# Kernel optimization log

Measured on AMD Instinct MI355X. Metric: run time of the kernel, lower is better.

The kernel has to match this reference:

```python
import jax, jax.numpy as jnp
import numpy as np

OUT_H, OUT_W, STRIDE = 100, 100, 4  # hardcoded in the torch module


def _downsample(pc):
    # pc: (B, 3, H, W) -> permute to (B, H, W, 3), strided-subsample, flatten to (B, N, 3)
    pc = jnp.transpose(pc, (0, 2, 3, 1))
    pc = pc[:, : OUT_H * STRIDE : STRIDE, : OUT_W * STRIDE : STRIDE, :]
    return pc.reshape(pc.shape[0], OUT_H * OUT_W, 3)


def setup_inputs() -> dict:
    key = jax.random.key(0)
    k1, k2 = jax.random.split(key)
    B, H, W = 4, 400, 400
    return {
        "target_pc": jax.random.normal(k1, (B, 3, H, W), dtype=jnp.float32),
        "source_pc": jax.random.normal(k2, (B, 3, H, W), dtype=jnp.float32),
    }


def reference(target_pc, source_pc):
    t = _downsample(target_pc)  # (B, N, 3) query points
    s = _downsample(source_pc)  # (B, N, 3) reference points
    # Squared Euclidean distances (B, Nt, Ns); argmin is identical for L2 vs L2^2.
    d2 = (
        jnp.sum(t * t, axis=-1)[:, :, None]
        + jnp.sum(s * s, axis=-1)[:, None, :]
        - 2.0 * jnp.einsum("bnd,bmd->bnm", t, s)
    )
    idx = jnp.argmin(d2, axis=-1)  # (B, Nt): nearest source index for each target point
    nearest = jnp.take_along_axis(s, idx[..., None], axis=1)  # (B, Nt, 3)
    per_batch = jnp.mean((nearest - t) ** 2, axis=(1, 2))  # MSE per batch element
    return jnp.mean(per_batch)
```

## Files before the change

### kernel.cpp

```cpp
#include <hip/hip_runtime.h>


#define BATCH  4
#define NPTS   10000
#define NPAD   10240
#define H      400
#define W      400
#define STRIDE 4
#define OUTW   100
#define NC     16
#define CHUNK  625
#define TBLKS  10
#define BLOCK  256
#define TPT    4

__global__ void prep_kernel(const float* __restrict__ tgt,
                            const float* __restrict__ src,
                            float4* __restrict__ S4,
                            float4* __restrict__ T4) {
    int gid = blockIdx.x * blockDim.x + threadIdx.x;
    if (gid < BATCH * NPAD) {
        int b = gid / NPAD;
        int n = gid % NPAD;
        float4 v = make_float4(0.f, 0.f, 0.f, 0.f);
        if (n < NPTS) {
            int h = n / OUTW, w = n % OUTW;
            int base = ((b * 3) * H + h * STRIDE) * W + w * STRIDE;
            float x = tgt[base];
            float y = tgt[base + H * W];
            float z = tgt[base + 2 * H * W];
            v = make_float4(x, y, z, x * x + y * y + z * z);
        }
        T4[gid] = v;
    } else {
        int sid = gid - BATCH * NPAD;
        if (sid < BATCH * NPTS) {
            int b = sid / NPTS;
            int m = sid % NPTS;
            int h = m / OUTW, w = m % OUTW;
            int base = ((b * 3) * H + h * STRIDE) * W + w * STRIDE;
            float x = src[base];
            float y = src[base + H * W];
            float z = src[base + 2 * H * W];
            S4[sid] = make_float4(-2.f * x, -2.f * y, -2.f * z,
                                  x * x + y * y + z * z);
        }
    }
}

__global__ __launch_bounds__(BLOCK) void knn_kernel(
        const float4* __restrict__ S4,
        const float4* __restrict__ T4,
        float* __restrict__ M2) {
    __shared__ float4 lds[CHUNK];
    const int tblk = blockIdx.x;
    const int cblk = blockIdx.y;
    const int b    = blockIdx.z;
    const int tid  = threadIdx.x;

    const float4* sbase = S4 + b * NPTS + cblk * CHUNK;
    for (int i = tid; i < CHUNK; i += BLOCK) lds[i] = sbase[i];

    const int tbase = b * NPAD + tblk * (BLOCK * TPT) + tid;
    float tx[TPT], ty[TPT], tz[TPT], mn[TPT];
#pragma unroll
    for (int k = 0; k < TPT; k++) {
        float4 t = T4[tbase + k * BLOCK];
        tx[k] = t.x; ty[k] = t.y; tz[k] = t.z;
        mn[k] = 3.0e38f;
    }
    __syncthreads();

#pragma unroll 5
    for (int j = 0; j < CHUNK; j++) {
        float4 s = lds[j];
#pragma unroll
        for (int k = 0; k < TPT; k++) {
            float d = fmaf(tx[k], s.x, s.w);
            d = fmaf(ty[k], s.y, d);
            d = fmaf(tz[k], s.z, d);
            mn[k] = fminf(mn[k], d);
        }
    }

    float* obase = M2 + (cblk * BATCH + b) * NPAD + tblk * (BLOCK * TPT) + tid;
#pragma unroll
    for (int k = 0; k < TPT; k++) obase[k * BLOCK] = mn[k];
}

__global__ void reduce_kernel(const float* __restrict__ M2,
                              const float4* __restrict__ T4,
                              float* __restrict__ out) {
    __shared__ float red[BLOCK / 64];
    int gid = blockIdx.x * BLOCK + threadIdx.x;
    float val = 0.f;
    if (gid < BATCH * NPTS) {
        int b = gid / NPTS;
        int n = gid % NPTS;
        float m = 3.0e38f;
#pragma unroll
        for (int c = 0; c < NC; c++)
            m = fminf(m, M2[(c * BATCH + b) * NPAD + n]);
        float tt = T4[b * NPAD + n].w;
        val = fmaxf(m + tt, 0.f);
    }
#pragma unroll
    for (int off = 32; off > 0; off >>= 1)
        val += __shfl_down(val, off, 64);
    int lane = threadIdx.x & 63;
    int wave = threadIdx.x >> 6;
    if (lane == 0) red[wave] = val;
    __syncthreads();
    if (threadIdx.x == 0) {
        float s = 0.f;
        for (int wv = 0; wv < BLOCK / 64; wv++) s += red[wv];
        atomicAdd(out, s * (1.0f / (BATCH * NPTS * 3)));
    }
}

extern "C" void kernel_launch(void* const* d_in, const int* in_sizes, int n_in,
                              void* d_out, int out_size, void* d_ws, size_t ws_size,
                              hipStream_t stream) {
    const float* tgt = (const float*)d_in[0];
    const float* src = (const float*)d_in[1];
    float* out = (float*)d_out;

    char* ws = (char*)d_ws;
    float4* S4 = (float4*)ws;
    float4* T4 = (float4*)(ws + (size_t)BATCH * NPTS * 16);
    float*  M2 = (float*)(ws + (size_t)BATCH * NPTS * 16
                             + (size_t)BATCH * NPAD * 16);

    hipMemsetAsync(out, 0, sizeof(float), stream);

    int nprep = BATCH * NPAD + BATCH * NPTS;
    prep_kernel<<<(nprep + 255) / 256, 256, 0, stream>>>(tgt, src, S4, T4);

    knn_kernel<<<dim3(TBLKS, NC, BATCH), BLOCK, 0, stream>>>(S4, T4, M2);

    reduce_kernel<<<(BATCH * NPTS + BLOCK - 1) / BLOCK, BLOCK, 0, stream>>>(
        M2, T4, out);
}
```

Baseline: 107.3 us.

## Restructure KNN inner loop with v_min3, 8 points per thread, prefetched LDS

New measurement: 122.6 us. 14.3% more time.

```diff
diff --git a/kernel.cpp b/kernel.cpp
--- a/kernel.cpp
+++ b/kernel.cpp
@@ -10,9 +10,17 @@
 #define OUTW   100
 #define NC     16
 #define CHUNK  625
-#define TBLKS  10
-#define BLOCK  256
-#define TPT    4
+#define CPAD   628
+#define KBLOCK 64
+#define TPT    8
+#define TBLKS  20
+#define RBLOCK 256
+
+__device__ __forceinline__ float min3f(float a, float b, float c) {
+    float r;
+    asm("v_min3_f32 %0, %1, %2, %3" : "=v"(r) : "v"(a), "v"(b), "v"(c));
+    return r;
+}
 
 __global__ void prep_kernel(const float* __restrict__ tgt,
                             const float* __restrict__ src,
@@ -48,51 +56,69 @@
     }
 }
 
-__global__ __launch_bounds__(BLOCK) void knn_kernel(
+#define COMPUTE4(q0, q1, q2, q3)                                   \
+    _Pragma("unroll")                                              \
+    for (int k = 0; k < TPT; k++) {                                \
+        float d0 = fmaf(tx[k], q0.x, q0.w);                        \
+        d0 = fmaf(ty[k], q0.y, d0);                                \
+        d0 = fmaf(tz[k], q0.z, d0);                                \
+        float d1 = fmaf(tx[k], q1.x, q1.w);                        \
+        d1 = fmaf(ty[k], q1.y, d1);                                \
+        d1 = fmaf(tz[k], q1.z, d1);                                \
+        float d2 = fmaf(tx[k], q2.x, q2.w);                        \
+        d2 = fmaf(ty[k], q2.y, d2);                                \
+        d2 = fmaf(tz[k], q2.z, d2);                                \
+        float d3 = fmaf(tx[k], q3.x, q3.w);                        \
+        d3 = fmaf(ty[k], q3.y, d3);                                \
+        d3 = fmaf(tz[k], q3.z, d3);                                \
+        mn[k] = min3f(mn[k], min3f(d0, d1, d2), d3);               \
+    }
+
+__global__ __launch_bounds__(KBLOCK) void knn_kernel(
         const float4* __restrict__ S4,
         const float4* __restrict__ T4,
         float* __restrict__ M2) {
-    __shared__ float4 lds[CHUNK];
+    __shared__ float4 lds[CPAD];
     const int tblk = blockIdx.x;
     const int cblk = blockIdx.y;
     const int b    = blockIdx.z;
     const int tid  = threadIdx.x;
 
     const float4* sbase = S4 + b * NPTS + cblk * CHUNK;
-    for (int i = tid; i < CHUNK; i += BLOCK) lds[i] = sbase[i];
+    for (int i = tid; i < CHUNK; i += KBLOCK) lds[i] = sbase[i];
+    if (tid < CPAD - CHUNK) lds[CHUNK + tid] = make_float4(0.f, 0.f, 0.f, 3.0e38f);
 
-    const int tbase = b * NPAD + tblk * (BLOCK * TPT) + tid;
+    const int tbase = b * NPAD + tblk * (KBLOCK * TPT) + tid;
     float tx[TPT], ty[TPT], tz[TPT], mn[TPT];
 #pragma unroll
     for (int k = 0; k < TPT; k++) {
-        float4 t = T4[tbase + k * BLOCK];
+        float4 t = T4[tbase + k * KBLOCK];
         tx[k] = t.x; ty[k] = t.y; tz[k] = t.z;
         mn[k] = 3.0e38f;
     }
     __syncthreads();
 
-#pragma unroll 5
-    for (int j = 0; j < CHUNK; j++) {
-        float4 s = lds[j];
+    float4 c0 = lds[0], c1 = lds[1], c2 = lds[2], c3 = lds[3];
+    for (int j = 4; j < CPAD; j += 4) {
+        float4 n0 = lds[j + 0];
+        float4 n1 = lds[j + 1];
+        float4 n2 = lds[j + 2];
+        float4 n3 = lds[j + 3];
+        COMPUTE4(c0, c1, c2, c3)
+        c0 = n0; c1 = n1; c2 = n2; c3 = n3;
+    }
+    COMPUTE4(c0, c1, c2, c3)
+
+    float* obase = M2 + (cblk * BATCH + b) * NPAD + tblk * (KBLOCK * TPT) + tid;
 #pragma unroll
-        for (int k = 0; k < TPT; k++) {
-            float d = fmaf(tx[k], s.x, s.w);
-            d = fmaf(ty[k], s.y, d);
-            d = fmaf(tz[k], s.z, d);
-            mn[k] = fminf(mn[k], d);
-        }
-    }
-
-    float* obase = M2 + (cblk * BATCH + b) * NPAD + tblk * (BLOCK * TPT) + tid;
-#pragma unroll
-    for (int k = 0; k < TPT; k++) obase[k * BLOCK] = mn[k];
+    for (int k = 0; k < TPT; k++) obase[k * KBLOCK] = mn[k];
 }
 
 __global__ void reduce_kernel(const float* __restrict__ M2,
                               const float4* __restrict__ T4,
                               float* __restrict__ out) {
-    __shared__ float red[BLOCK / 64];
-    int gid = blockIdx.x * BLOCK + threadIdx.x;
+    __shared__ float red[RBLOCK / 64];
+    int gid = blockIdx.x * RBLOCK + threadIdx.x;
     float val = 0.f;
     if (gid < BATCH * NPTS) {
         int b = gid / NPTS;
@@ -113,7 +139,7 @@
     __syncthreads();
     if (threadIdx.x == 0) {
         float s = 0.f;
-        for (int wv = 0; wv < BLOCK / 64; wv++) s += red[wv];
+        for (int wv = 0; wv < RBLOCK / 64; wv++) s += red[wv];
         atomicAdd(out, s * (1.0f / (BATCH * NPTS * 3)));
     }
 }
@@ -134,10 +160,10 @@
     hipMemsetAsync(out, 0, sizeof(float), stream);
 
     int nprep = BATCH * NPAD + BATCH * NPTS;
-    prep_kernel<<<(nprep + 255) / 256, 256, 0, stream>>>(tgt, src, S4, T4);
+    prep_kernel<<<(nprep + RBLOCK - 1) / RBLOCK, RBLOCK, 0, stream>>>(tgt, src, S4, T4);
 
-    knn_kernel<<<dim3(TBLKS, NC, BATCH), BLOCK, 0, stream>>>(S4, T4, M2);
+    knn_kernel<<<dim3(TBLKS, NC, BATCH), KBLOCK, 0, stream>>>(S4, T4, M2);
 
-    reduce_kernel<<<(BATCH * NPTS + BLOCK - 1) / BLOCK, BLOCK, 0, stream>>>(
+    reduce_kernel<<<(BATCH * NPTS + RBLOCK - 1) / RBLOCK, RBLOCK, 0, stream>>>(
         M2, T4, out);
 }
```

## Drop LDS staging, read padded source chunks directly, use min3 with more targets per thread

Applied to the files above, without the earlier changes.

Result: slower. 124.5 us (+16.0%).

```diff
diff --git a/kernel.cpp b/kernel.cpp
--- a/kernel.cpp
+++ b/kernel.cpp
@@ -8,11 +8,19 @@
 #define W      400
 #define STRIDE 4
 #define OUTW   100
-#define NC     16
-#define CHUNK  625
-#define TBLKS  10
+#define NC     64
+#define CHUNK  157
+#define CPAD   160
 #define BLOCK  256
-#define TPT    4
+#define TPT    8
+#define TBLKS  5
+#define RBLOCK 256
+
+__device__ __forceinline__ float min3f(float a, float b, float c) {
+    float r;
+    asm("v_min3_f32 %0, %1, %2, %3" : "=v"(r) : "v"(a), "v"(b), "v"(c));
+    return r;
+}
 
 __global__ void prep_kernel(const float* __restrict__ tgt,
                             const float* __restrict__ src,
@@ -34,16 +42,23 @@
         T4[gid] = v;
     } else {
         int sid = gid - BATCH * NPAD;
-        if (sid < BATCH * NPTS) {
-            int b = sid / NPTS;
-            int m = sid % NPTS;
-            int h = m / OUTW, w = m % OUTW;
-            int base = ((b * 3) * H + h * STRIDE) * W + w * STRIDE;
-            float x = src[base];
-            float y = src[base + H * W];
-            float z = src[base + 2 * H * W];
-            S4[sid] = make_float4(-2.f * x, -2.f * y, -2.f * z,
-                                  x * x + y * y + z * z);
+        if (sid < BATCH * NC * CPAD) {
+            int b = sid / (NC * CPAD);
+            int r = sid % (NC * CPAD);
+            int c = r / CPAD;
+            int i = r % CPAD;
+            int m = c * CHUNK + i;
+            float4 v = make_float4(0.f, 0.f, 0.f, 3.0e38f);
+            if (i < CHUNK && m < NPTS) {
+                int h = m / OUTW, w = m % OUTW;
+                int base = ((b * 3) * H + h * STRIDE) * W + w * STRIDE;
+                float x = src[base];
+                float y = src[base + H * W];
+                float z = src[base + 2 * H * W];
+                v = make_float4(-2.f * x, -2.f * y, -2.f * z,
+                                x * x + y * y + z * z);
+            }
+            S4[sid] = v;
         }
     }
 }
@@ -52,14 +67,12 @@
         const float4* __restrict__ S4,
         const float4* __restrict__ T4,
         float* __restrict__ M2) {
-    __shared__ float4 lds[CHUNK];
     const int tblk = blockIdx.x;
     const int cblk = blockIdx.y;
     const int b    = blockIdx.z;
     const int tid  = threadIdx.x;
 
-    const float4* sbase = S4 + b * NPTS + cblk * CHUNK;
-    for (int i = tid; i < CHUNK; i += BLOCK) lds[i] = sbase[i];
+    const float4* sbase = S4 + (size_t)(b * NC + cblk) * CPAD;
 
     const int tbase = b * NPAD + tblk * (BLOCK * TPT) + tid;
     float tx[TPT], ty[TPT], tz[TPT], mn[TPT];
@@ -69,21 +82,33 @@
         tx[k] = t.x; ty[k] = t.y; tz[k] = t.z;
         mn[k] = 3.0e38f;
     }
-    __syncthreads();
 
-#pragma unroll 5
-    for (int j = 0; j < CHUNK; j++) {
-        float4 s = lds[j];
+    for (int j = 0; j < CPAD; j += 4) {
+        float4 sa = sbase[j + 0];
+        float4 sb = sbase[j + 1];
+        float4 sc = sbase[j + 2];
+        float4 sd = sbase[j + 3];
 #pragma unroll
         for (int k = 0; k < TPT; k++) {
-            float d = fmaf(tx[k], s.x, s.w);
-            d = fmaf(ty[k], s.y, d);
-            d = fmaf(tz[k], s.z, d);
-            mn[k] = fminf(mn[k], d);
+            float da = fmaf(tx[k], sa.x, sa.w);
+            da = fmaf(ty[k], sa.y, da);
+            da = fmaf(tz[k], sa.z, da);
+            float db = fmaf(tx[k], sb.x, sb.w);
+            db = fmaf(ty[k], sb.y, db);
+            db = fmaf(tz[k], sb.z, db);
+            float dc = fmaf(tx[k], sc.x, sc.w);
+            dc = fmaf(ty[k], sc.y, dc);
+            dc = fmaf(tz[k], sc.z, dc);
+            float dd = fmaf(tx[k], sd.x, sd.w);
+            dd = fmaf(ty[k], sd.y, dd);
+            dd = fmaf(tz[k], sd.z, dd);
+            mn[k] = min3f(mn[k], da, db);
+            mn[k] = min3f(mn[k], dc, dd);
         }
     }
 
-    float* obase = M2 + (cblk * BATCH + b) * NPAD + tblk * (BLOCK * TPT) + tid;
+    float* obase = M2 + (size_t)(cblk * BATCH + b) * NPAD
+                      + tblk * (BLOCK * TPT) + tid;
 #pragma unroll
     for (int k = 0; k < TPT; k++) obase[k * BLOCK] = mn[k];
 }
@@ -91,16 +116,16 @@
 __global__ void reduce_kernel(const float* __restrict__ M2,
                               const float4* __restrict__ T4,
                               float* __restrict__ out) {
-    __shared__ float red[BLOCK / 64];
-    int gid = blockIdx.x * BLOCK + threadIdx.x;
+    __shared__ float red[RBLOCK / 64];
+    int gid = blockIdx.x * RBLOCK + threadIdx.x;
     float val = 0.f;
     if (gid < BATCH * NPTS) {
         int b = gid / NPTS;
         int n = gid % NPTS;
         float m = 3.0e38f;
-#pragma unroll
+#pragma unroll 8
         for (int c = 0; c < NC; c++)
-            m = fminf(m, M2[(c * BATCH + b) * NPAD + n]);
+            m = fminf(m, M2[(size_t)(c * BATCH + b) * NPAD + n]);
         float tt = T4[b * NPAD + n].w;
         val = fmaxf(m + tt, 0.f);
     }
@@ -113,7 +138,7 @@
     __syncthreads();
     if (threadIdx.x == 0) {
         float s = 0.f;
-        for (int wv = 0; wv < BLOCK / 64; wv++) s += red[wv];
+        for (int wv = 0; wv < RBLOCK / 64; wv++) s += red[wv];
         atomicAdd(out, s * (1.0f / (BATCH * NPTS * 3)));
     }
 }
@@ -127,17 +152,17 @@
 
     char* ws = (char*)d_ws;
     float4* S4 = (float4*)ws;
-    float4* T4 = (float4*)(ws + (size_t)BATCH * NPTS * 16);
-    float*  M2 = (float*)(ws + (size_t)BATCH * NPTS * 16
+    float4* T4 = (float4*)(ws + (size_t)BATCH * NC * CPAD * 16);
+    float*  M2 = (float*)(ws + (size_t)BATCH * NC * CPAD * 16
                              + (size_t)BATCH * NPAD * 16);
 
     hipMemsetAsync(out, 0, sizeof(float), stream);
 
-    int nprep = BATCH * NPAD + BATCH * NPTS;
-    prep_kernel<<<(nprep + 255) / 256, 256, 0, stream>>>(tgt, src, S4, T4);
+    int nprep = BATCH * NPAD + BATCH * NC * CPAD;
+    prep_kernel<<<(nprep + RBLOCK - 1) / RBLOCK, RBLOCK, 0, stream>>>(tgt, src, S4, T4);
 
     knn_kernel<<<dim3(TBLKS, NC, BATCH), BLOCK, 0, stream>>>(S4, T4, M2);
 
-    reduce_kernel<<<(BATCH * NPTS + BLOCK - 1) / BLOCK, BLOCK, 0, stream>>>(
+    reduce_kernel<<<(BATCH * NPTS + RBLOCK - 1) / RBLOCK, RBLOCK, 0, stream>>>(
         M2, T4, out);
 }
```

## Compute pairwise distances with bf16 MFMA using split-precision packing

Applied to the files above, without the earlier changes.

New measurement: 117.1 us. 9.1% more time.

```diff
diff --git a/kernel.cpp b/kernel.cpp
--- a/kernel.cpp
+++ b/kernel.cpp
@@ -1,4 +1,5 @@
 #include <hip/hip_runtime.h>
+#include <hip/hip_bf16.h>
 
 
 #define BATCH  4
@@ -8,99 +9,154 @@
 #define W      400
 #define STRIDE 4
 #define OUTW   100
-#define NC     16
-#define CHUNK  625
-#define TBLKS  10
-#define BLOCK  256
-#define TPT    4
+#define NCH    4
+#define CCOLS  (NPAD / NCH)
+#define CTILES (CCOLS / 32)
+#define MT     128
+#define RBLOCK 256
+
+typedef short short8 __attribute__((ext_vector_type(8)));
+typedef float f32x16 __attribute__((ext_vector_type(16)));
+
+__device__ __forceinline__ unsigned short f2bf(float x) {
+    __hip_bfloat16 h = __float2bfloat16(x);
+    return *reinterpret_cast<unsigned short*>(&h);
+}
+__device__ __forceinline__ float bf2f(unsigned short u) {
+    __hip_bfloat16 h = *reinterpret_cast<__hip_bfloat16*>(&u);
+    return __bfloat162float(h);
+}
 
 __global__ void prep_kernel(const float* __restrict__ tgt,
                             const float* __restrict__ src,
-                            float4* __restrict__ S4,
+                            unsigned short* __restrict__ A_pack,
+                            unsigned short* __restrict__ B_pack,
                             float4* __restrict__ T4) {
     int gid = blockIdx.x * blockDim.x + threadIdx.x;
     if (gid < BATCH * NPAD) {
-        int b = gid / NPAD;
-        int n = gid % NPAD;
-        float4 v = make_float4(0.f, 0.f, 0.f, 0.f);
+        int b = gid / NPAD, n = gid % NPAD;
+        unsigned short a[16];
+#pragma unroll
+        for (int i = 0; i < 16; i++) a[i] = 0;
+        float4 tv = make_float4(0.f, 0.f, 0.f, 0.f);
         if (n < NPTS) {
             int h = n / OUTW, w = n % OUTW;
             int base = ((b * 3) * H + h * STRIDE) * W + w * STRIDE;
             float x = tgt[base];
             float y = tgt[base + H * W];
             float z = tgt[base + 2 * H * W];
-            v = make_float4(x, y, z, x * x + y * y + z * z);
+            tv = make_float4(x, y, z, x * x + y * y + z * z);
+            unsigned short th0 = f2bf(x), th1 = f2bf(y), th2 = f2bf(z);
+            a[0] = th0; a[1] = th1; a[2] = th2;
+            a[3] = th0; a[4] = th1; a[5] = th2;
+            a[6] = f2bf(x - bf2f(th0));
+            a[7] = f2bf(y - bf2f(th1));
+            a[8] = f2bf(z - bf2f(th2));
+            a[9] = f2bf(1.0f); a[10] = f2bf(1.0f);
         }
-        T4[gid] = v;
+        T4[gid] = tv;
+        uint4* dst = (uint4*)(A_pack + (size_t)gid * 16);
+        dst[0] = *(uint4*)&a[0];
+        dst[1] = *(uint4*)&a[8];
     } else {
         int sid = gid - BATCH * NPAD;
-        if (sid < BATCH * NPTS) {
-            int b = sid / NPTS;
-            int m = sid % NPTS;
-            int h = m / OUTW, w = m % OUTW;
-            int base = ((b * 3) * H + h * STRIDE) * W + w * STRIDE;
-            float x = src[base];
-            float y = src[base + H * W];
-            float z = src[base + 2 * H * W];
-            S4[sid] = make_float4(-2.f * x, -2.f * y, -2.f * z,
-                                  x * x + y * y + z * z);
+        if (sid < BATCH * NPAD) {
+            int b = sid / NPAD, n = sid % NPAD;
+            unsigned short v[16];
+#pragma unroll
+            for (int i = 0; i < 16; i++) v[i] = 0;
+            if (n < NPTS) {
+                int h = n / OUTW, w = n % OUTW;
+                int base = ((b * 3) * H + h * STRIDE) * W + w * STRIDE;
+                float x = src[base];
+                float y = src[base + H * W];
+                float z = src[base + 2 * H * W];
+                float ss = x * x + y * y + z * z;
+                float v0 = -2.f * x, v1 = -2.f * y, v2 = -2.f * z;
+                unsigned short vh0 = f2bf(v0), vh1 = f2bf(v1), vh2 = f2bf(v2);
+                v[0] = vh0; v[1] = vh1; v[2] = vh2;
+                v[3] = f2bf(v0 - bf2f(vh0));
+                v[4] = f2bf(v1 - bf2f(vh1));
+                v[5] = f2bf(v2 - bf2f(vh2));
+                v[6] = vh0; v[7] = vh1; v[8] = vh2;
+                unsigned short sh = f2bf(ss);
+                v[9] = sh; v[10] = f2bf(ss - bf2f(sh));
+            } else {
+                v[9] = f2bf(1.0e30f);
+            }
+            uint4* dst = (uint4*)(B_pack + (size_t)sid * 16);
+            dst[0] = *(uint4*)&v[0];
+            dst[1] = *(uint4*)&v[8];
         }
     }
 }
 
-__global__ __launch_bounds__(BLOCK) void knn_kernel(
-        const float4* __restrict__ S4,
-        const float4* __restrict__ T4,
+__global__ __launch_bounds__(RBLOCK) void knn_kernel(
+        const unsigned short* __restrict__ A_pack,
+        const unsigned short* __restrict__ B_pack,
         float* __restrict__ M2) {
-    __shared__ float4 lds[CHUNK];
-    const int tblk = blockIdx.x;
-    const int cblk = blockIdx.y;
-    const int b    = blockIdx.z;
-    const int tid  = threadIdx.x;
-
-    const float4* sbase = S4 + b * NPTS + cblk * CHUNK;
-    for (int i = tid; i < CHUNK; i += BLOCK) lds[i] = sbase[i];
-
-    const int tbase = b * NPAD + tblk * (BLOCK * TPT) + tid;
-    float tx[TPT], ty[TPT], tz[TPT], mn[TPT];
-#pragma unroll
-    for (int k = 0; k < TPT; k++) {
-        float4 t = T4[tbase + k * BLOCK];
-        tx[k] = t.x; ty[k] = t.y; tz[k] = t.z;
-        mn[k] = 3.0e38f;
-    }
-    __syncthreads();
-
-#pragma unroll 5
-    for (int j = 0; j < CHUNK; j++) {
-        float4 s = lds[j];
-#pragma unroll
-        for (int k = 0; k < TPT; k++) {
-            float d = fmaf(tx[k], s.x, s.w);
-            d = fmaf(ty[k], s.y, d);
-            d = fmaf(tz[k], s.z, d);
-            mn[k] = fminf(mn[k], d);
+    const int wave = threadIdx.x >> 6;
+    const int lane = threadIdx.x & 63;
+    const int l31  = lane & 31;
+    const int half = lane >> 5;
+    const int b      = blockIdx.z;
+    const int cchunk = blockIdx.y;
+    const int r0     = blockIdx.x * MT + wave * 32;
+
+    union { uint4 u; short8 s; } af, bf, bn;
+    af.u = *(const uint4*)(A_pack + ((size_t)b * NPAD + r0 + l31) * 16 + half * 8);
+
+    const unsigned short* bbase =
+        B_pack + ((size_t)b * NPAD + (size_t)cchunk * CCOLS + l31) * 16 + half * 8;
+
+    float rmin[16];
+#pragma unroll
+    for (int r = 0; r < 16; r++) rmin[r] = 3.0e38f;
+
+    bf.u = *(const uint4*)bbase;
+    for (int ct = 0; ct < CTILES; ct++) {
+        if (ct + 1 < CTILES)
+            bn.u = *(const uint4*)(bbase + (size_t)(ct + 1) * 32 * 16);
+        f32x16 z = {};
+        f32x16 acc = __builtin_amdgcn_mfma_f32_32x32x16_bf16(af.s, bf.s, z, 0, 0, 0);
+#pragma unroll
+        for (int r = 0; r < 16; r++) rmin[r] = fminf(rmin[r], acc[r]);
+        bf.u = bn.u;
+    }
+
+#pragma unroll
+    for (int r = 0; r < 16; r++) {
+        float v = rmin[r];
+        v = fminf(v, __shfl_xor(v, 1, 64));
+        v = fminf(v, __shfl_xor(v, 2, 64));
+        v = fminf(v, __shfl_xor(v, 4, 64));
+        v = fminf(v, __shfl_xor(v, 8, 64));
+        v = fminf(v, __shfl_xor(v, 16, 64));
+        rmin[r] = v;
+    }
+    if (l31 == 0) {
+        float* o = M2 + ((size_t)cchunk * BATCH + b) * NPAD + r0;
+#pragma unroll
+        for (int r = 0; r < 16; r++) {
+            int row = (r & 3) + 8 * (r >> 2) + 4 * half;
+            o[row] = rmin[r];
         }
     }
-
-    float* obase = M2 + (cblk * BATCH + b) * NPAD + tblk * (BLOCK * TPT) + tid;
-#pragma unroll
-    for (int k = 0; k < TPT; k++) obase[k * BLOCK] = mn[k];
 }
 
 __global__ void reduce_kernel(const float* __restrict__ M2,
                               const float4* __restrict__ T4,
                               float* __restrict__ out) {
-    __shared__ float red[BLOCK / 64];
-    int gid = blockIdx.x * BLOCK + threadIdx.x;
+    __shared__ float red[RBLOCK / 64];
+    int gid = blockIdx.x * RBLOCK + threadIdx.x;
     float val = 0.f;
     if (gid < BATCH * NPTS) {
         int b = gid / NPTS;
         int n = gid % NPTS;
         float m = 3.0e38f;
 #pragma unroll
-        for (int c = 0; c < NC; c++)
-            m = fminf(m, M2[(c * BATCH + b) * NPAD + n]);
+        for (int c = 0; c < NCH; c++)
+            m = fminf(m, M2[((size_t)c * BATCH + b) * NPAD + n]);
         float tt = T4[b * NPAD + n].w;
         val = fmaxf(m + tt, 0.f);
     }
@@ -113,7 +169,7 @@
     __syncthreads();
     if (threadIdx.x == 0) {
         float s = 0.f;
-        for (int wv = 0; wv < BLOCK / 64; wv++) s += red[wv];
+        for (int wv = 0; wv < RBLOCK / 64; wv++) s += red[wv];
         atomicAdd(out, s * (1.0f / (BATCH * NPTS * 3)));
     }
 }
@@ -126,18 +182,21 @@
     float* out = (float*)d_out;
 
     char* ws = (char*)d_ws;
-    float4* S4 = (float4*)ws;
-    float4* T4 = (float4*)(ws + (size_t)BATCH * NPTS * 16);
-    float*  M2 = (float*)(ws + (size_t)BATCH * NPTS * 16
+    unsigned short* A_pack = (unsigned short*)ws;
+    unsigned short* B_pack = (unsigned short*)(ws + (size_t)BATCH * NPAD * 32);
+    float4* T4 = (float4*)(ws + (size_t)BATCH * NPAD * 64);
+    float*  M2 = (float*)(ws + (size_t)BATCH * NPAD * 64
                              + (size_t)BATCH * NPAD * 16);
 
     hipMemsetAsync(out, 0, sizeof(float), stream);
 
-    int nprep = BATCH * NPAD + BATCH * NPTS;
-    prep_kernel<<<(nprep + 255) / 256, 256, 0, stream>>>(tgt, src, S4, T4);
-
-    knn_kernel<<<dim3(TBLKS, NC, BATCH), BLOCK, 0, stream>>>(S4, T4, M2);
-
-    reduce_kernel<<<(BATCH * NPTS + BLOCK - 1) / BLOCK, BLOCK, 0, stream>>>(
+    int nprep = 2 * BATCH * NPAD;
+    prep_kernel<<<(nprep + RBLOCK - 1) / RBLOCK, RBLOCK, 0, stream>>>(
+        tgt, src, A_pack, B_pack, T4);
+
+    knn_kernel<<<dim3(NPAD / MT, NCH, BATCH), RBLOCK, 0, stream>>>(
+        A_pack, B_pack, M2);
+
+    reduce_kernel<<<(BATCH * NPTS + RBLOCK - 1) / RBLOCK, RBLOCK, 0, stream>>>(
         M2, T4, out);
 }
```
